# Kernel optimization log

Hardware: AMD Instinct MI355X
Metric: run time of the kernel (lower is better)

Reference implementation:

```python
import jax, jax.numpy as jnp
import numpy as np

ALPHA = 0.2  # leaky relu slope
DEPTH = 3
MAX_REF = 10
MAX_DIR = 32

def leaky(x):
    return jnp.where(x >= 0, x, ALPHA * x)

def setup_inputs() -> dict:
    key = jax.random.key(0)
    ks = jax.random.split(key, 9)
    N, F_IN, F_OUT = 100000, 128, 128
    h = jax.random.normal(ks[0], (N, F_IN), dtype=jnp.float32)
    W_ref = jax.random.normal(ks[1], (F_IN, F_OUT), dtype=jnp.float32) * 0.1
    a_ref = jax.random.normal(ks[2], (2 * F_OUT, 1), dtype=jnp.float32) * 0.1
    W_dir = jax.random.normal(ks[3], (F_IN, F_OUT), dtype=jnp.float32) * 0.1
    a_dir = jax.random.normal(ks[4], (2 * F_OUT, 1), dtype=jnp.float32) * 0.1
    ref_neighbors = jax.random.randint(ks[5], (N, DEPTH + 1, MAX_REF), 0, N)
    ref_counts = jax.random.randint(ks[6], (N, DEPTH + 1), 0, MAX_REF + 1)
    dir_neighbors = jax.random.randint(ks[7], (N, MAX_DIR), 0, N)
    dir_counts = jax.random.randint(ks[8], (N,), 1, MAX_DIR + 1)
    return {"h": h, "W_ref": W_ref, "a_ref": a_ref, "W_dir": W_dir, "a_dir": a_dir,
            "ref_neighbors": ref_neighbors, "ref_counts": ref_counts,
            "dir_neighbors": dir_neighbors, "dir_counts": dir_counts}

def _forward_ref(h, W_ref, a_ref, ref_neighbors, ref_counts):
    Wh = h @ W_ref                                  # [N, F]
    F_ = Wh.shape[1]
    # mean of (up to 10) neighbor features per (node, depth); empty -> zeros
    nbr = Wh[ref_neighbors]                         # [N, D+1, 10, F]
    slot = jnp.arange(MAX_REF)[None, None, :]
    valid = slot < ref_counts[:, :, None]           # [N, D+1, 10]
    cnt = jnp.maximum(ref_counts, 1).astype(Wh.dtype)  # avoid div by 0
    f_ref = jnp.einsum('ndkf,ndk->ndf', nbr, valid.astype(Wh.dtype)) / cnt[:, :, None]  # [N, D+1, F]
    # attention score: leaky(cat(Wh[node], f_ref[d]) @ a_ref)
    a_self, a_nbr = a_ref[:F_, 0], a_ref[F_:, 0]
    e = leaky(Wh @ a_self[:, None] + f_ref @ a_nbr)  # [N,1]+[N,D+1] -> [N, D+1]
    alpha = jax.nn.softmax(e, axis=-1)
    out = jnp.einsum('ndf,nd->nf', f_ref, alpha)
    return jax.nn.sigmoid(out)

def _forward_dir(h, W_dir, a_dir, dir_neighbors, dir_counts):
    Wh = h @ W_dir                                  # [N, F]
    F_ = Wh.shape[1]
    nbr = Wh[dir_neighbors]                         # [N, K, F]
    a_self, a_nbr = a_dir[:F_, 0], a_dir[F_:, 0]
    e = leaky((Wh @ a_self)[:, None] + nbr @ a_nbr)  # [N, K]
    valid = jnp.arange(MAX_DIR)[None, :] < dir_counts[:, None]
    e = jnp.where(valid, e, -jnp.inf)
    alpha = jax.nn.softmax(e, axis=-1)
    out = jnp.einsum('nkf,nk->nf', nbr, alpha)
    return jax.nn.sigmoid(out)

def reference(h, W_ref, a_ref, W_dir, a_dir, ref_neighbors, ref_counts, dir_neighbors, dir_counts):
    h_ref = _forward_ref(h, W_ref, a_ref, ref_neighbors, ref_counts)
    h_dir = _forward_dir(h, W_dir, a_dir, dir_neighbors, dir_counts)
    return (h_ref + h_dir) / 2  # mode='mean'
```

## Files before the change

kernel.cpp:

```cpp
#include <hip/hip_runtime.h>

typedef __attribute__((ext_vector_type(8))) short s16x8;
typedef __attribute__((ext_vector_type(4))) float f32x4;
typedef __attribute__((ext_vector_type(2))) float f32x2;

#define F 128

__device__ __forceinline__ unsigned short f2bf(float f) {
    unsigned int u = __float_as_uint(f);
    u = (u + 0x7fffu + ((u >> 16) & 1u)) >> 16;
    return (unsigned short)u;
}
__device__ __forceinline__ float bflo(unsigned int u) { return __uint_as_float(u << 16); }
__device__ __forceinline__ float bfhi(unsigned int u) { return __uint_as_float(u & 0xffff0000u); }
__device__ __forceinline__ float leaky(float x) { return x >= 0.f ? x : 0.2f * x; }
__device__ __forceinline__ float sigmoidf(float x) { return 1.f / (1.f + __expf(-x)); }

#define SWZ16(row, b) ((b) ^ (((row) & 7) << 4))

#define WAVE_LDS_FENCE() do { \
    asm volatile("s_waitcnt lgkmcnt(0)" ::: "memory"); \
    __builtin_amdgcn_sched_barrier(0); \
} while (0)

__device__ __forceinline__ void glds16(void* lds, const void* g) {
    __builtin_amdgcn_global_load_lds(
        (const __attribute__((address_space(1))) unsigned int*)g,
        (__attribute__((address_space(3))) unsigned int*)lds,
        16, 0, 0);
}

__global__ __launch_bounds__(256) void prep_w(const float* __restrict__ wRef,
                                              const float* __restrict__ wDir,
                                              unsigned short* __restrict__ wT) {
    int i = blockIdx.x * 256 + threadIdx.x;
    int m = i >> 14;
    int rr = i & 16383;
    int k = rr >> 7;
    int c = rr & 127;
    const float* W = m ? wDir : wRef;
    wT[m * 16384 + c * 128 + (k ^ (((c & 7) << 3)))] = f2bf(W[k * 128 + c]);
}

__device__ __forceinline__ void epi(const f32x4* acc, unsigned char* cb ,
                                    int rowBase, int w, int r, int g, int lane, int N,
                                    const float* __restrict__ aVec,
                                    unsigned char* __restrict__ wh ,
                                    float* __restrict__ sArr, float* __restrict__ tArr) {
    float ps[4] = {0.f, 0.f, 0.f, 0.f}, pt[4] = {0.f, 0.f, 0.f, 0.f};
#pragma unroll
    for (int ct = 0; ct < 8; ++ct) {
        int c = ct * 16 + r;
        float As = aVec[c], At = aVec[128 + c];
#pragma unroll
        for (int q = 0; q < 4; ++q) { ps[q] += acc[ct][q] * As; pt[q] += acc[ct][q] * At; }
    }
#pragma unroll
    for (int off = 1; off <= 8; off <<= 1) {
#pragma unroll
        for (int q = 0; q < 4; ++q) {
            ps[q] += __shfl_xor(ps[q], off);
            pt[q] += __shfl_xor(pt[q], off);
        }
    }
    if (r == 0) {
#pragma unroll
        for (int q = 0; q < 4; ++q) {
            int row = rowBase + w * 16 + g * 4 + q;
            if (row < N) { sArr[row] = ps[q]; tArr[row] = pt[q]; }
        }
    }
#pragma unroll
    for (int ct = 0; ct < 8; ++ct) {
#pragma unroll
        for (int q = 0; q < 4; ++q) {
            int lrow = g * 4 + q;
            int xb = (ct * 16 + r) * 2;
            *(unsigned short*)(cb + lrow * 256 + SWZ16(lrow, xb)) = f2bf(acc[ct][q]);
        }
    }
#pragma unroll
    for (int i = 0; i < 4; ++i) {
        int off = i * 1024 + lane * 16;
        int lrow = off >> 8, x = off & 255;
        uint4 v = *(const uint4*)(cb + lrow * 256 + SWZ16(lrow, x));
        int pk0 = __builtin_amdgcn_cvt_pk_fp8_f32(bflo(v.x), bfhi(v.x), 0, false);
        pk0 = __builtin_amdgcn_cvt_pk_fp8_f32(bflo(v.y), bfhi(v.y), pk0, true);
        int pk1 = __builtin_amdgcn_cvt_pk_fp8_f32(bflo(v.z), bfhi(v.z), 0, false);
        pk1 = __builtin_amdgcn_cvt_pk_fp8_f32(bflo(v.w), bfhi(v.w), pk1, true);
        int grow = rowBase + w * 16 + lrow;
        if (grow < N) *(uint2*)(wh + (size_t)grow * 128 + (x >> 1)) = make_uint2((unsigned)pk0, (unsigned)pk1);
    }
}

__global__ __launch_bounds__(256) void gemm_wh(const float* __restrict__ h,
                                               const unsigned short* __restrict__ wT,
                                               const float* __restrict__ aRefG,
                                               const float* __restrict__ aDirG,
                                               unsigned char* __restrict__ whRef,
                                               unsigned char* __restrict__ whDir,
                                               float* __restrict__ sRef, float* __restrict__ tRef,
                                               float* __restrict__ sDir, float* __restrict__ tDir,
                                               int N) {
    __shared__ unsigned char lds[49152];
    const int tid = threadIdx.x;
    const int lane = tid & 63, w = tid >> 6;
    const int r = lane & 15, g = lane >> 4;
    const int rowBase = blockIdx.x * 64;

#pragma unroll
    for (int it = 0; it < 8; ++it) {
        int lin = it * 4096 + tid * 16;
        glds16(lds + 16384 + lin, (const char*)wT + lin);
    }
    float4 av[4][2];
#pragma unroll
    for (int it = 0; it < 4; ++it) {
        int lin = it * 4096 + tid * 16;
        int arow = lin >> 8, x = lin & 255;
        int grow = min(rowBase + arow, N - 1);
        const char* src = (const char*)h + (size_t)grow * 512 + x * 2;
        av[it][0] = *(const float4*)(src);
        av[it][1] = *(const float4*)(src + 16);
    }
#pragma unroll
    for (int it = 0; it < 4; ++it) {
        int lin = it * 4096 + tid * 16;
        int arow = lin >> 8, x = lin & 255;
        s16x8 a;
        a[0] = (short)f2bf(av[it][0].x); a[1] = (short)f2bf(av[it][0].y);
        a[2] = (short)f2bf(av[it][0].z); a[3] = (short)f2bf(av[it][0].w);
        a[4] = (short)f2bf(av[it][1].x); a[5] = (short)f2bf(av[it][1].y);
        a[6] = (short)f2bf(av[it][1].z); a[7] = (short)f2bf(av[it][1].w);
        *(s16x8*)(lds + arow * 256 + SWZ16(arow, x)) = a;
    }
    __syncthreads();

    s16x8 afr[4];
    {
        const int arow = w * 16 + r;
#pragma unroll
        for (int kt = 0; kt < 4; ++kt)
            afr[kt] = *(const s16x8*)(lds + arow * 256 + SWZ16(arow, kt * 64 + g * 16));
    }
    unsigned char* cb = lds + w * 4096;

    {
        f32x4 acc[8];
#pragma unroll
        for (int ct = 0; ct < 8; ++ct) acc[ct] = (f32x4){0.f, 0.f, 0.f, 0.f};
#pragma unroll
        for (int kt = 0; kt < 4; ++kt) {
#pragma unroll
            for (int ct = 0; ct < 8; ++ct) {
                int c = ct * 16 + r;
                s16x8 b = *(const s16x8*)(lds + 16384 + c * 256 + SWZ16(c, kt * 64 + g * 16));
                acc[ct] = __builtin_amdgcn_mfma_f32_16x16x32_bf16(afr[kt], b, acc[ct], 0, 0, 0);
            }
        }
        epi(acc, cb, rowBase, w, r, g, lane, N, aRefG, whRef, sRef, tRef);
    }
    __syncthreads();
#pragma unroll
    for (int it = 0; it < 8; ++it) {
        int lin = it * 4096 + tid * 16;
        glds16(lds + 16384 + lin, (const char*)wT + 32768 + lin);
    }
    __syncthreads();
    {
        f32x4 acc[8];
#pragma unroll
        for (int ct = 0; ct < 8; ++ct) acc[ct] = (f32x4){0.f, 0.f, 0.f, 0.f};
#pragma unroll
        for (int kt = 0; kt < 4; ++kt) {
#pragma unroll
            for (int ct = 0; ct < 8; ++ct) {
                int c = ct * 16 + r;
                s16x8 b = *(const s16x8*)(lds + 16384 + c * 256 + SWZ16(c, kt * 64 + g * 16));
                acc[ct] = __builtin_amdgcn_mfma_f32_16x16x32_bf16(afr[kt], b, acc[ct], 0, 0, 0);
            }
        }
        epi(acc, cb, rowBase, w, r, g, lane, N, aDirG, whDir, sDir, tDir);
    }
}

__device__ __forceinline__ void acc8f8(float* a, uint2 u, float c) {
    f32x2 p0 = __builtin_amdgcn_cvt_pk_f32_fp8((int)u.x, false);
    f32x2 p1 = __builtin_amdgcn_cvt_pk_f32_fp8((int)u.x, true);
    f32x2 p2 = __builtin_amdgcn_cvt_pk_f32_fp8((int)u.y, false);
    f32x2 p3 = __builtin_amdgcn_cvt_pk_f32_fp8((int)u.y, true);
    a[0] += c * p0[0]; a[1] += c * p0[1];
    a[2] += c * p1[0]; a[3] += c * p1[1];
    a[4] += c * p2[0]; a[5] += c * p2[1];
    a[6] += c * p3[0]; a[7] += c * p3[1];
}

__global__ __launch_bounds__(256) void gather_attn(
    const unsigned char* __restrict__ whRef, const unsigned char* __restrict__ whDir,
    const float* __restrict__ sRef, const float* __restrict__ tRef,
    const float* __restrict__ sDir, const float* __restrict__ tDir,
    const int* __restrict__ refNbr, const int* __restrict__ refCnt,
    const int* __restrict__ dirNbr, const int* __restrict__ dirCnt,
    float* __restrict__ out, int N) {
    __shared__ int   s_idx[4][72];
    __shared__ float s_coef[4][72];

    const int wid = threadIdx.x >> 6;
    const int lane = threadIdx.x & 63;
    const int q = lane >> 4, hl16 = lane & 15;
    const int d = lane >> 4, kk = lane & 15;
    const int n_raw = blockIdx.x * 4 + wid;
    const int n = min(n_raw, N - 1);

    int cnt = refCnt[n * 4 + d];
    int idxR = (kk < 10) ? refNbr[(size_t)n * 40 + d * 10 + kk] : 0;
    int dcnt = dirCnt[n];
    int idxD = (lane < 32) ? dirNbr[(size_t)n * 32 + lane] : 0;
    float sR = sRef[n], sD = sDir[n];

    bool validR = kk < cnt;
    unsigned long long mask = __ballot(validR);
    int pos = (int)__popcll(mask & ((1ull << lane) - 1ull));
    int Lr = (int)__popcll(mask);
    if (validR) s_idx[wid][pos] = idxR;
    if (lane < 32) s_idx[wid][40 + lane] = idxD;
    WAVE_LDS_FENCE();

    uint2 uR[10];
#pragma unroll
    for (int j = 0; j < 10; ++j) {
        int e = j * 4 + q;
        if (e < Lr)
            uR[j] = *(const uint2*)(whRef + ((size_t)(unsigned)s_idx[wid][e] << 7) + (hl16 << 3));
    }
    uint2 uD[8];
#pragma unroll
    for (int j = 0; j < 8; ++j) {
        int e = j * 4 + q;
        if (e < dcnt)
            uD[j] = *(const uint2*)(whDir + ((size_t)(unsigned)s_idx[wid][40 + e] << 7) + (hl16 << 3));
    }

    float tv = validR ? tRef[idxR] : 0.f;
    float sum = tv;
    sum += __shfl_xor(sum, 1); sum += __shfl_xor(sum, 2);
    sum += __shfl_xor(sum, 4); sum += __shfl_xor(sum, 8);
    float rc = 1.f / (float)max(cnt, 1);
    float e = leaky(sR + sum * rc);
    float mx = fmaxf(e, __shfl_xor(e, 16)); mx = fmaxf(mx, __shfl_xor(mx, 32));
    float wgt = __expf(e - mx);
    float den = wgt + __shfl_xor(wgt, 16); den += __shfl_xor(den, 32);
    float coefR = wgt / den * rc;
    if (validR) s_coef[wid][pos] = coefR;

    float eD = -1e30f;
    float tD = (lane < 32 && lane < dcnt) ? tDir[idxD] : 0.f;
    if (lane < 32 && lane < dcnt) eD = leaky(sD + tD);
    float mD = eD;
#pragma unroll
    for (int off = 16; off; off >>= 1) mD = fmaxf(mD, __shfl_xor(mD, off, 32));
    float wD = (lane < dcnt) ? __expf(eD - mD) : 0.f;
    float dD = wD;
#pragma unroll
    for (int off = 16; off; off >>= 1) dD += __shfl_xor(dD, off, 32);
    if (lane < 32 && lane < dcnt) s_coef[wid][40 + lane] = wD / dD;
    WAVE_LDS_FENCE();

    float accR[8] = {0.f, 0.f, 0.f, 0.f, 0.f, 0.f, 0.f, 0.f};
#pragma unroll
    for (int j = 0; j < 10; ++j) {
        int e = j * 4 + q;
        if (e < Lr) acc8f8(accR, uR[j], s_coef[wid][e]);
    }
    float accD[8] = {0.f, 0.f, 0.f, 0.f, 0.f, 0.f, 0.f, 0.f};
#pragma unroll
    for (int j = 0; j < 8; ++j) {
        int e = j * 4 + q;
        if (e < dcnt) acc8f8(accD, uD[j], s_coef[wid][40 + e]);
    }

#pragma unroll
    for (int j = 0; j < 8; ++j) {
        accR[j] += __shfl_xor(accR[j], 16); accR[j] += __shfl_xor(accR[j], 32);
        accD[j] += __shfl_xor(accD[j], 16); accD[j] += __shfl_xor(accD[j], 32);
    }
    if (n_raw < N && q == 0) {
        float o[8];
#pragma unroll
        for (int j = 0; j < 8; ++j) o[j] = 0.5f * (sigmoidf(accR[j]) + sigmoidf(accD[j]));
        float4* dst = (float4*)(out + (size_t)n * F + hl16 * 8);
        dst[0] = make_float4(o[0], o[1], o[2], o[3]);
        dst[1] = make_float4(o[4], o[5], o[6], o[7]);
    }
}

extern "C" void kernel_launch(void* const* d_in, const int* in_sizes, int n_in,
                              void* d_out, int out_size, void* d_ws, size_t ws_size,
                              hipStream_t stream) {
    const float* h    = (const float*)d_in[0];
    const float* Wref = (const float*)d_in[1];
    const float* aRef = (const float*)d_in[2];
    const float* Wdir = (const float*)d_in[3];
    const float* aDir = (const float*)d_in[4];
    const int* refNbr = (const int*)d_in[5];
    const int* refCnt = (const int*)d_in[6];
    const int* dirNbr = (const int*)d_in[7];
    const int* dirCnt = (const int*)d_in[8];
    float* out = (float*)d_out;
    const int N = in_sizes[0] / F;

    const size_t NF = (size_t)N * F;
    unsigned char* whRef = (unsigned char*)d_ws;
    unsigned char* whDir = whRef + NF;
    float* sRef = (float*)(whDir + NF);
    float* tRef = sRef + N;
    float* sDir = tRef + N;
    float* tDir = sDir + N;
    unsigned short* wT = (unsigned short*)(tDir + N);

    prep_w<<<128, 256, 0, stream>>>(Wref, Wdir, wT);
    gemm_wh<<<(N + 63) / 64, 256, 0, stream>>>(h, wT, aRef, aDir, whRef, whDir,
                                               sRef, tRef, sDir, tDir, N);
    gather_attn<<<(N + 3) / 4, 256, 0, stream>>>(whRef, whDir, sRef, tRef, sDir, tDir,
                                                 refNbr, refCnt, dirNbr, dirCnt, out, N);
}
```

Measured before the change: 246.0 us.

## Stage gathered neighbor rows into LDS via async global_load_lds

The gather kernel now copies neighbor feature rows into a per-wave LDS staging buffer with global_load_lds, 16 bytes per lane, instead of loading 8-byte chunks into registers. Loops run only up to the actual neighbor counts, and the softmax math overlaps the in-flight loads before a vmcnt wait. The accumulation switches to packed FMA instructions. This cuts register pressure and uses wider, more coalesced loads, but adds about 37KB of LDS per block, which may limit occupancy.

```diff
diff --git a/kernel.cpp b/kernel.cpp
--- a/kernel.cpp
+++ b/kernel.cpp
@@ -20,6 +20,11 @@
 
 #define WAVE_LDS_FENCE() do { \
     asm volatile("s_waitcnt lgkmcnt(0)" ::: "memory"); \
+    __builtin_amdgcn_sched_barrier(0); \
+} while (0)
+
+#define AWAIT_VM0() do { \
+    asm volatile("s_waitcnt vmcnt(0)" ::: "memory"); \
     __builtin_amdgcn_sched_barrier(0); \
 } while (0)
 
@@ -28,6 +33,17 @@
         (const __attribute__((address_space(1))) unsigned int*)g,
         (__attribute__((address_space(3))) unsigned int*)lds,
         16, 0, 0);
+}
+
+__device__ __forceinline__ void pkfma(f32x2& a, f32x2 p, f32x2 cc) {
+    asm("v_pk_fma_f32 %0, %1, %2, %0" : "+v"(a) : "v"(p), "v"(cc));
+}
+__device__ __forceinline__ void accrow(f32x2* a4, uint2 u, float c) {
+    f32x2 cc; cc[0] = c; cc[1] = c;
+    pkfma(a4[0], __builtin_amdgcn_cvt_pk_f32_fp8((int)u.x, false), cc);
+    pkfma(a4[1], __builtin_amdgcn_cvt_pk_f32_fp8((int)u.x, true),  cc);
+    pkfma(a4[2], __builtin_amdgcn_cvt_pk_f32_fp8((int)u.y, false), cc);
+    pkfma(a4[3], __builtin_amdgcn_cvt_pk_f32_fp8((int)u.y, true),  cc);
 }
 
 __global__ __launch_bounds__(256) void prep_w(const float* __restrict__ wRef,
@@ -42,10 +58,10 @@
     wT[m * 16384 + c * 128 + (k ^ (((c & 7) << 3)))] = f2bf(W[k * 128 + c]);
 }
 
-__device__ __forceinline__ void epi(const f32x4* acc, unsigned char* cb ,
+__device__ __forceinline__ void epi(const f32x4* acc, unsigned char* cb,
                                     int rowBase, int w, int r, int g, int lane, int N,
                                     const float* __restrict__ aVec,
-                                    unsigned char* __restrict__ wh ,
+                                    unsigned char* __restrict__ wh,
                                     float* __restrict__ sArr, float* __restrict__ tArr) {
     float ps[4] = {0.f, 0.f, 0.f, 0.f}, pt[4] = {0.f, 0.f, 0.f, 0.f};
 #pragma unroll
@@ -184,17 +200,6 @@
     }
 }
 
-__device__ __forceinline__ void acc8f8(float* a, uint2 u, float c) {
-    f32x2 p0 = __builtin_amdgcn_cvt_pk_f32_fp8((int)u.x, false);
-    f32x2 p1 = __builtin_amdgcn_cvt_pk_f32_fp8((int)u.x, true);
-    f32x2 p2 = __builtin_amdgcn_cvt_pk_f32_fp8((int)u.y, false);
-    f32x2 p3 = __builtin_amdgcn_cvt_pk_f32_fp8((int)u.y, true);
-    a[0] += c * p0[0]; a[1] += c * p0[1];
-    a[2] += c * p1[0]; a[3] += c * p1[1];
-    a[4] += c * p2[0]; a[5] += c * p2[1];
-    a[6] += c * p3[0]; a[7] += c * p3[1];
-}
-
 __global__ __launch_bounds__(256) void gather_attn(
     const unsigned char* __restrict__ whRef, const unsigned char* __restrict__ whDir,
     const float* __restrict__ sRef, const float* __restrict__ tRef,
@@ -202,6 +207,7 @@
     const int* __restrict__ refNbr, const int* __restrict__ refCnt,
     const int* __restrict__ dirNbr, const int* __restrict__ dirCnt,
     float* __restrict__ out, int N) {
+    __shared__ unsigned char s_stage[4][9216];
     __shared__ int   s_idx[4][72];
     __shared__ float s_coef[4][72];
 
@@ -211,6 +217,10 @@
     const int d = lane >> 4, kk = lane & 15;
     const int n_raw = blockIdx.x * 4 + wid;
     const int n = min(n_raw, N - 1);
+    unsigned char* stg = s_stage[wid];
+
+    s_idx[wid][lane] = 0;
+    if (lane < 8) s_idx[wid][64 + lane] = 0;
 
     int cnt = refCnt[n * 4 + d];
     int idxR = (kk < 10) ? refNbr[(size_t)n * 40 + d * 10 + kk] : 0;
@@ -219,66 +229,86 @@
     float sR = sRef[n], sD = sDir[n];
 
     bool validR = kk < cnt;
+    bool validD = (lane < 32) && (lane < dcnt);
+    float rc = 1.f / (float)max(cnt, 1);
     unsigned long long mask = __ballot(validR);
     int pos = (int)__popcll(mask & ((1ull << lane) - 1ull));
     int Lr = (int)__popcll(mask);
+    WAVE_LDS_FENCE();
     if (validR) s_idx[wid][pos] = idxR;
-    if (lane < 32) s_idx[wid][40 + lane] = idxD;
+    if (validD) s_idx[wid][40 + lane] = idxD;
+
+    float tv = validR ? tRef[idxR] : 0.f;
+    float tD = validD ? tDir[idxD] : 0.f;
     WAVE_LDS_FENCE();
 
-    uint2 uR[10];
-#pragma unroll
-    for (int j = 0; j < 10; ++j) {
-        int e = j * 4 + q;
-        if (e < Lr)
-            uR[j] = *(const uint2*)(whRef + ((size_t)(unsigned)s_idx[wid][e] << 7) + (hl16 << 3));
-    }
-    uint2 uD[8];
-#pragma unroll
-    for (int j = 0; j < 8; ++j) {
-        int e = j * 4 + q;
-        if (e < dcnt)
-            uD[j] = *(const uint2*)(whDir + ((size_t)(unsigned)s_idx[wid][40 + e] << 7) + (hl16 << 3));
-    }
-
-    float tv = validR ? tRef[idxR] : 0.f;
+    const int nR8 = (Lr + 7) >> 3;
+    const int nD8 = (dcnt + 7) >> 3;
+    const int sub = (lane >> 3);
+    const int seg = (lane & 7) << 4;
+    for (int j = 0; j < nR8; ++j) {
+        int row = s_idx[wid][j * 8 + sub];
+        glds16(stg + j * 1024 + lane * 16,
+               whRef + ((size_t)(unsigned)row << 7) + seg);
+    }
+    for (int j = 0; j < nD8; ++j) {
+        int row = s_idx[wid][40 + j * 8 + sub];
+        glds16(stg + 5120 + j * 1024 + lane * 16,
+               whDir + ((size_t)(unsigned)row << 7) + seg);
+    }
+    __builtin_amdgcn_sched_barrier(0);
+
     float sum = tv;
     sum += __shfl_xor(sum, 1); sum += __shfl_xor(sum, 2);
     sum += __shfl_xor(sum, 4); sum += __shfl_xor(sum, 8);
-    float rc = 1.f / (float)max(cnt, 1);
     float e = leaky(sR + sum * rc);
     float mx = fmaxf(e, __shfl_xor(e, 16)); mx = fmaxf(mx, __shfl_xor(mx, 32));
     float wgt = __expf(e - mx);
     float den = wgt + __shfl_xor(wgt, 16); den += __shfl_xor(den, 32);
-    float coefR = wgt / den * rc;
-    if (validR) s_coef[wid][pos] = coefR;
-
-    float eD = -1e30f;
-    float tD = (lane < 32 && lane < dcnt) ? tDir[idxD] : 0.f;
-    if (lane < 32 && lane < dcnt) eD = leaky(sD + tD);
+    if (validR) s_coef[wid][pos] = wgt / den * rc;
+
+    float eD = validD ? leaky(sD + tD) : -1e30f;
     float mD = eD;
 #pragma unroll
     for (int off = 16; off; off >>= 1) mD = fmaxf(mD, __shfl_xor(mD, off, 32));
-    float wD = (lane < dcnt) ? __expf(eD - mD) : 0.f;
+    float wD = validD ? __expf(eD - mD) : 0.f;
     float dD = wD;
 #pragma unroll
     for (int off = 16; off; off >>= 1) dD += __shfl_xor(dD, off, 32);
-    if (lane < 32 && lane < dcnt) s_coef[wid][40 + lane] = wD / dD;
+    if (validD) s_coef[wid][40 + lane] = wD / dD;
     WAVE_LDS_FENCE();
 
-    float accR[8] = {0.f, 0.f, 0.f, 0.f, 0.f, 0.f, 0.f, 0.f};
-#pragma unroll
-    for (int j = 0; j < 10; ++j) {
-        int e = j * 4 + q;
-        if (e < Lr) acc8f8(accR, uR[j], s_coef[wid][e]);
-    }
-    float accD[8] = {0.f, 0.f, 0.f, 0.f, 0.f, 0.f, 0.f, 0.f};
-#pragma unroll
-    for (int j = 0; j < 8; ++j) {
-        int e = j * 4 + q;
-        if (e < dcnt) acc8f8(accD, uD[j], s_coef[wid][40 + e]);
-    }
-
+    AWAIT_VM0();
+
+    f32x2 aR[4] = {{0.f,0.f},{0.f,0.f},{0.f,0.f},{0.f,0.f}};
+    {
+        int mR = (Lr + 3) >> 2;
+        for (int j = 0; j < mR; ++j) {
+            int e2 = j * 4 + q;
+            if (e2 < Lr) {
+                uint2 u = *(const uint2*)(stg + e2 * 128 + (hl16 << 3));
+                accrow(aR, u, s_coef[wid][e2]);
+            }
+        }
+    }
+    f32x2 aD4[4] = {{0.f,0.f},{0.f,0.f},{0.f,0.f},{0.f,0.f}};
+    {
+        int mD4 = (dcnt + 3) >> 2;
+        for (int j = 0; j < mD4; ++j) {
+            int e2 = j * 4 + q;
+            if (e2 < dcnt) {
+                uint2 u = *(const uint2*)(stg + 5120 + e2 * 128 + (hl16 << 3));
+                accrow(aD4, u, s_coef[wid][40 + e2]);
+            }
+        }
+    }
+
+    float accR[8], accD[8];
+#pragma unroll
+    for (int j = 0; j < 4; ++j) {
+        accR[2*j] = aR[j][0]; accR[2*j+1] = aR[j][1];
+        accD[2*j] = aD4[j][0]; accD[2*j+1] = aD4[j][1];
+    }
 #pragma unroll
     for (int j = 0; j < 8; ++j) {
         accR[j] += __shfl_xor(accR[j], 16); accR[j] += __shfl_xor(accR[j], 32);
```

Result: slower. 288.8 us (+17.4%).
